# Kernel optimization log

Measured on AMD Instinct MI355X. Metric: run time of the kernel, lower is better.

## Reference

```python
import jax, jax.numpy as jnp
import numpy as np

WS = 11        # gaussian window size
SIGMA = 1.5    # gaussian sigma
L = 10.0       # val_range
SSIM_C1 = (0.01 * L) ** 2
SSIM_C2 = (0.03 * L) ** 2


def _window():
    g = jnp.exp(-((jnp.arange(WS) - WS // 2) ** 2) / (2.0 * SIGMA ** 2))
    g = g / g.sum()
    return jnp.outer(g, g).astype(jnp.float32)  # [11,11], sums to 1


def _blur(z, win):
    # depthwise 11x11 gaussian blur with VALID padding; z: [..., H, W]
    lead = z.shape[:-2]
    zf = z.reshape((-1, 1) + z.shape[-2:])
    out = jax.lax.conv_general_dilated(zf, win[None, None], (1, 1), 'VALID')
    return out.reshape(lead + out.shape[-2:])


def setup_inputs() -> dict:
    key = jax.random.key(0)
    ks = jax.random.split(key, 7)
    B, C, Fc, H, W = 8, 64, 3, 192, 192
    return {
        'x': jax.random.normal(ks[0], (B, C, H, W), jnp.float32),
        'x_feature': jax.random.normal(ks[1], (B, Fc, H, W), jnp.float32),
        'spatial_w': jax.random.normal(ks[2], (1, Fc, 3, 1), jnp.float32) * 0.1,
        'W1': jax.random.normal(ks[3], (C, C), jnp.float32) * 0.05,
        'b1': jnp.zeros((C,), jnp.float32),
        'W2': jax.random.normal(ks[4], (C, C), jnp.float32) * 0.05,
        'b2': jnp.zeros((C,), jnp.float32),
    }


def reference(x, x_feature, spatial_w, W1, b1, W2, b2):
    win = _window()
    # per-channel gaussian moments (computed once, reused across all pairs)
    mu_x = _blur(x, win)                         # [B,C,h,w]
    mu_f = _blur(x_feature, win)                 # [B,F,h,w]
    sig_x = _blur(x * x, win) - mu_x ** 2        # variance of x channels
    sig_f = _blur(x_feature * x_feature, win) - mu_f ** 2
    # all pairwise cross-covariances in one batched blur
    prod = x_feature[:, :, None] * x[:, None]    # [B,F,C,H,W]
    sig_fx = _blur(prod, win) - mu_f[:, :, None] * mu_x[:, None]
    v1 = 2.0 * sig_fx + SSIM_C2
    v2 = sig_f[:, :, None] + sig_x[:, None] + SSIM_C2
    num = (2.0 * mu_f[:, :, None] * mu_x[:, None] + SSIM_C1) * v1
    den = (mu_f[:, :, None] ** 2 + mu_x[:, None] ** 2 + SSIM_C1) * v2
    ssim_info = (num / den).mean(axis=(-2, -1))  # [B,F,C]
    # spatial gate: Conv2d(3,1,(3,1),padding=(1,0)) over [B,F,C,1]
    si4 = ssim_info[..., None]                   # [B,F,C,1]
    h = jax.lax.conv_general_dilated(si4, spatial_w, (1, 1), ((1, 1), (0, 0)))
    h = jax.nn.relu(h).reshape(x.shape[0], -1)   # [B,C]
    h = jax.nn.relu(h @ W1.T + b1) @ W2.T + b2
    return jax.nn.sigmoid(h), ssim_info
```

## Files before the change

### kernel.cpp

```cpp
#include <hip/hip_runtime.h>
#include <math.h>

#define HW 192
#define OW 182
#define NPIX (OW*OW)
#define NTILE 8
#define SSIM_C1 0.01f
#define SSIM_C2 0.09f

#define Gk0 0.0010283835f
#define Gk1 0.0075987615f
#define Gk2 0.0360007700f
#define Gk3 0.1093608000f
#define Gk4 0.2130055400f
#define Gk5 0.2660117000f

typedef float v2f __attribute__((ext_vector_type(2)));

__device__ __forceinline__ v2f vfma(float w, v2f a, v2f b) {
    return __builtin_elementwise_fma((v2f){w, w}, a, b);
}
__device__ __forceinline__ v2f vfma2(v2f w, v2f a, v2f b) {
    return __builtin_elementwise_fma(w, a, b);
}

__device__ __forceinline__ void dgauss(float g[11]) {
    float s = 0.f;
#pragma unroll
    for (int i = 0; i < 11; ++i) {
        float d = (float)(i - 5);
        g[i] = expf(-(d * d) / 4.5f);
        s += g[i];
    }
    float inv = 1.f / s;
#pragma unroll
    for (int i = 0; i < 11; ++i) g[i] *= inv;
}

__global__ __launch_bounds__(256) void muf_kernel(const float* __restrict__ xf,
                                                  float* __restrict__ muf,
                                                  float* __restrict__ sigc2f) {
    const int tile = blockIdx.x % 14;
    const int img  = blockIdx.x / 14;
    const int r0   = tile * 13;

    __shared__ float raw[23][192];
    __shared__ float hb[2][23][184];

    float g[11]; dgauss(g);
    const int t = threadIdx.x;
    const float* src = xf + (size_t)img * HW * HW;

    for (int i = t; i < 23 * 192; i += 256) {
        int rr = i / 192, col = i - rr * 192;
        raw[rr][col] = src[(r0 + rr) * HW + col];
    }
    __syncthreads();

    for (int i = t; i < 23 * OW; i += 256) {
        int rr = i / OW, co = i - rr * OW;
        float a0 = 0.f, a1 = 0.f;
#pragma unroll
        for (int k = 0; k < 11; ++k) {
            float v = raw[rr][co + k];
            float w = g[k];
            a0 += w * v;
            a1 += w * v * v;
        }
        hb[0][rr][co] = a0;
        hb[1][rr][co] = a1;
    }
    __syncthreads();

    for (int i = t; i < 13 * OW; i += 256) {
        int rr = i / OW, co = i - rr * OW;
        float m = 0.f, s2 = 0.f;
#pragma unroll
        for (int k = 0; k < 11; ++k) {
            float w = g[k];
            m  += w * hb[0][rr + k][co];
            s2 += w * hb[1][rr + k][co];
        }
        size_t o = (size_t)img * NPIX + (size_t)(r0 + rr) * OW + co;
        muf[o]    = m;
        sigc2f[o] = s2 - m * m + SSIM_C2;
    }
}

__global__ __launch_bounds__(192, 4) void ssim_kernel(const float* __restrict__ x,
                                                      const float* __restrict__ xf,
                                                      const float* __restrict__ muf,
                                                      const float* __restrict__ sigc2f,
                                                      float* __restrict__ part) {
    const float G[11] = {Gk0,Gk1,Gk2,Gk3,Gk4,Gk5,Gk4,Gk3,Gk2,Gk1,Gk0};
    const v2f WA[6] = {{G[0],0.f},{G[2],G[1]},{G[4],G[3]},{G[6],G[5]},{G[8],G[7]},{G[10],G[9]}};
    const v2f WB[6] = {{G[1],G[0]},{G[3],G[2]},{G[5],G[4]},{G[7],G[6]},{G[9],G[8]},{0.f,G[10]}};

    const int blk  = blockIdx.x;
    const int c    = blk & 63;
    const int tile = (blk >> 6) & 7;
    const int b    = blk >> 9;

    const int out0  = (tile * 182) >> 3;
    const int out1  = ((tile + 1) * 182) >> 3;
    const int n_out = out1 - out0;

    const int t    = threadIdx.x;
    const int half = (t >= 96) ? 1 : 0;
    const int u    = half ? (t - 96) : t;
    const int cu   = 2 * u;
    const bool act = (u <= 90);

    const float* xp  = x  + ((size_t)(b * 64 + c)) * HW * HW + (size_t)out0 * HW + t;
    const float* fp0 = xf + ((size_t)(b * 3 + 0)) * HW * HW + (size_t)out0 * HW + t;
    const float* fp1 = fp0 + HW * HW;
    const float* fp2 = fp1 + HW * HW;

    const float* mp = muf    + (size_t)(b * 3) * NPIX + (size_t)(out0 + half) * OW + cu;
    const float* cp = sigc2f + (size_t)(b * 3) * NPIX + (size_t)(out0 + half) * OW + cu;

    __shared__ float eb[4][5][192];
    __shared__ float red[3][3];

    v2f P01[10], P23[10];
    float P4[10];
#pragma unroll
    for (int j = 0; j < 10; ++j) { P01[j] = (v2f){0.f,0.f}; P23[j] = (v2f){0.f,0.f}; P4[j] = 0.f; }

    v2f A0 = {0.f,0.f}, A1 = {0.f,0.f}, A2 = {0.f,0.f};

    v2f eE01, eE23; float eE4;

    auto vstep = [&](float xv, float a0, float a1, float a2, bool emit) {
        v2f v01 = {xv, xv * xv};
        v2f v23 = {xv * a0, xv * a1};
        float v4 = xv * a2;
        if (emit) {
            eE01 = vfma(G[10], v01, P01[0]);
            eE23 = vfma(G[10], v23, P23[0]);
            eE4  = fmaf(G[10], v4, P4[0]);
        }
#pragma unroll
        for (int j = 0; j < 9; ++j) {
            P01[j] = vfma(G[9 - j], v01, P01[j + 1]);
            P23[j] = vfma(G[9 - j], v23, P23[j + 1]);
            P4[j]  = fmaf(G[9 - j], v4, P4[j + 1]);
        }
        P01[9] = G[0] * v01;
        P23[9] = G[0] * v23;
        P4[9]  = G[0] * v4;
    };

    auto ssim2 = [&](const v2f mux, const v2f mux2, const v2f sigc,
                     const v2f mf, const v2f cc, const v2f h, v2f& A) {
        v2f t1  = mf * mux;
        v2f sfx = h - t1;
        v2f v1s = vfma(2.f, sfx, (v2f){SSIM_C2, SSIM_C2});
        v2f n1  = vfma(2.f, t1, (v2f){SSIM_C1, SSIM_C1});
        v2f num = n1 * v1s;
        v2f qd  = vfma2(mf, mf, (v2f){SSIM_C1, SSIM_C1});
        v2f den = (qd + mux2) * (cc + sigc);
        v2f inv = {__builtin_amdgcn_rcpf(den.x), __builtin_amdgcn_rcpf(den.y)};
        A = vfma2(num, inv, A);
    };

    auto store_e = [&](int slot) {
        eb[slot][0][t] = eE01.x; eb[slot][1][t] = eE01.y;
        eb[slot][2][t] = eE23.x; eb[slot][3][t] = eE23.y;
        eb[slot][4][t] = eE4;
    };

#pragma unroll 1
    for (int r = 0; r < 10; r += 2) {
        float xA0 = xp[0],  a00 = fp0[0],  a10 = fp1[0],  a20 = fp2[0];
        float xB0 = xp[HW], b00 = fp0[HW], b10 = fp1[HW], b20 = fp2[HW];
        xp += 2 * HW; fp0 += 2 * HW; fp1 += 2 * HW; fp2 += 2 * HW;
        vstep(xA0, a00, a10, a20, false);
        vstep(xB0, b00, b10, b20, false);
    }

    const int n_pair = n_out >> 1;

    float xA = xp[0],  aA0 = fp0[0],  aA1 = fp1[0],  aA2 = fp2[0];
    float xB = xp[HW], aB0 = fp0[HW], aB1 = fp1[HW], aB2 = fp2[HW];
    xp += 2 * HW; fp0 += 2 * HW; fp1 += 2 * HW; fp2 += 2 * HW;
    float yA = xp[0],  bA0 = fp0[0],  bA1 = fp1[0],  bA2 = fp2[0];
    float yB = xp[HW], bB0 = fp0[HW], bB1 = fp1[HW], bB2 = fp2[HW];
    xp += 2 * HW; fp0 += 2 * HW; fp1 += 2 * HW; fp2 += 2 * HW;

#pragma unroll 1
    for (int p = 0; p < n_pair; ++p) {
        const int rb = 2 * p + 4;
        const int o1 = ((rb     < n_out) ? 0 : (n_out - 1 - rb)) * HW;
        const int o2 = ((rb + 1 < n_out) ? 1 : (n_out - 1 - rb)) * HW;
        const float nxA = xp[o1], nA0 = fp0[o1], nA1 = fp1[o1], nA2 = fp2[o1];
        const float nxB = xp[o2], nB0 = fp0[o2], nB1 = fp1[o2], nB2 = fp2[o2];
        xp += 2 * HW; fp0 += 2 * HW; fp1 += 2 * HW; fp2 += 2 * HW;

        v2f mf0, mf1, mf2, cc0, cc1, cc2;
        if (act) {
            mf0 = *(const v2f*)(mp);
            mf1 = *(const v2f*)(mp + NPIX);
            mf2 = *(const v2f*)(mp + 2 * NPIX);
            cc0 = *(const v2f*)(cp);
            cc1 = *(const v2f*)(cp + NPIX);
            cc2 = *(const v2f*)(cp + 2 * NPIX);
            mp += 2 * OW; cp += 2 * OW;
        }

        const int e = 2 * p;
        const int sA = e & 3, sB = (e + 1) & 3;
        vstep(xA, aA0, aA1, aA2, true);  store_e(sA);
        vstep(xB, aB0, aB1, aB2, true);  store_e(sB);
        __syncthreads();

        xA = yA;  aA0 = bA0; aA1 = bA1; aA2 = bA2;
        xB = yB;  aB0 = bB0; aB1 = bB1; aB2 = bB2;
        yA = nxA; bA0 = nA0; bA1 = nA1; bA2 = nA2;
        yB = nxB; bB0 = nB0; bB1 = nB1; bB2 = nB2;

        if (act) {
            const int sH = half ? sB : sA;
            v2f hacc[5];
#pragma unroll
            for (int f = 0; f < 5; ++f) {
                const float* ep = &eb[sH][f][cu];
                v2f a = {0.f, 0.f};
#pragma unroll
                for (int m = 0; m < 6; ++m) {
                    v2f rd = *(const v2f*)(ep + 2 * m);
                    a = vfma2(WA[m], __builtin_shufflevector(rd, rd, 0, 0), a);
                    a = vfma2(WB[m], __builtin_shufflevector(rd, rd, 1, 1), a);
                }
                hacc[f] = a;
            }
            const v2f mux  = hacc[0];
            const v2f mux2 = mux * mux;
            const v2f sigc = hacc[1] - mux2;
            ssim2(mux, mux2, sigc, mf0, cc0, hacc[2], A0);
            ssim2(mux, mux2, sigc, mf1, cc1, hacc[3], A1);
            ssim2(mux, mux2, sigc, mf2, cc2, hacc[4], A2);
        }
    }

    if (n_out & 1) {
        const int e = n_out - 1;
        vstep(xA, aA0, aA1, aA2, true);
        const int sA = e & 3;
        store_e(sA);
        __syncthreads();
        if (act && half == 0) {
            v2f mf0 = *(const v2f*)(mp);
            v2f mf1 = *(const v2f*)(mp + NPIX);
            v2f mf2 = *(const v2f*)(mp + 2 * NPIX);
            v2f cc0 = *(const v2f*)(cp);
            v2f cc1 = *(const v2f*)(cp + NPIX);
            v2f cc2 = *(const v2f*)(cp + 2 * NPIX);
            v2f hacc[5];
#pragma unroll
            for (int f = 0; f < 5; ++f) {
                const float* ep = &eb[sA][f][cu];
                v2f a = {0.f, 0.f};
#pragma unroll
                for (int m = 0; m < 6; ++m) {
                    v2f rd = *(const v2f*)(ep + 2 * m);
                    a = vfma2(WA[m], __builtin_shufflevector(rd, rd, 0, 0), a);
                    a = vfma2(WB[m], __builtin_shufflevector(rd, rd, 1, 1), a);
                }
                hacc[f] = a;
            }
            const v2f mux  = hacc[0];
            const v2f mux2 = mux * mux;
            const v2f sigc = hacc[1] - mux2;
            ssim2(mux, mux2, sigc, mf0, cc0, hacc[2], A0);
            ssim2(mux, mux2, sigc, mf1, cc1, hacc[3], A1);
            ssim2(mux, mux2, sigc, mf2, cc2, hacc[4], A2);
        }
    }

    float acc0 = A0.x + A0.y;
    float acc1 = A1.x + A1.y;
    float acc2 = A2.x + A2.y;
#pragma unroll
    for (int off = 32; off > 0; off >>= 1) {
        acc0 += __shfl_down(acc0, off);
        acc1 += __shfl_down(acc1, off);
        acc2 += __shfl_down(acc2, off);
    }
    const int wid = t >> 6, lane = t & 63;
    if (lane == 0) { red[0][wid] = acc0; red[1][wid] = acc1; red[2][wid] = acc2; }
    __syncthreads();
    if (t == 0) {
        const size_t o = (size_t)tile * 1536 + (size_t)b * 192;
        part[o +   0 + c] = red[0][0] + red[0][1] + red[0][2];
        part[o +  64 + c] = red[1][0] + red[1][1] + red[1][2];
        part[o + 128 + c] = red[2][0] + red[2][1] + red[2][2];
    }
}

__global__ __launch_bounds__(64) void gate_kernel(const float* __restrict__ part,
                                                  const float* __restrict__ sw,
                                                  const float* __restrict__ W1,
                                                  const float* __restrict__ b1,
                                                  const float* __restrict__ W2,
                                                  const float* __restrict__ b2,
                                                  float* __restrict__ out,
                                                  float* __restrict__ out_ssim) {
    const int b = blockIdx.x;
    const int c = threadIdx.x;

    __shared__ float s[3][64];
    __shared__ float h0[64];
    __shared__ float h1[64];

    const float inv = 1.f / (float)NPIX;
#pragma unroll
    for (int f = 0; f < 3; ++f) {
        const int i = b * 192 + f * 64 + c;
        float v = 0.f;
#pragma unroll
        for (int k = 0; k < NTILE; ++k) v += part[i + k * 1536];
        v *= inv;
        s[f][c] = v;
        out_ssim[i] = v;
    }
    __syncthreads();

    float a = 0.f;
#pragma unroll
    for (int f = 0; f < 3; ++f)
#pragma unroll
        for (int i = 0; i < 3; ++i) {
            int cc = c - 1 + i;
            if (cc >= 0 && cc < 64) a += sw[f * 3 + i] * s[f][cc];
        }
    h0[c] = fmaxf(a, 0.f);
    __syncthreads();

    float a1 = b1[c];
    for (int j = 0; j < 64; ++j) a1 += W1[c * 64 + j] * h0[j];
    h1[c] = fmaxf(a1, 0.f);
    __syncthreads();

    float a2 = b2[c];
    for (int j = 0; j < 64; ++j) a2 += W2[c * 64 + j] * h1[j];
    out[b * 64 + c] = 1.f / (1.f + expf(-a2));
}

extern "C" void kernel_launch(void* const* d_in, const int* in_sizes, int n_in,
                              void* d_out, int out_size, void* d_ws, size_t ws_size,
                              hipStream_t stream) {
    const float* x  = (const float*)d_in[0];
    const float* xf = (const float*)d_in[1];
    const float* sw = (const float*)d_in[2];
    const float* W1 = (const float*)d_in[3];
    const float* b1 = (const float*)d_in[4];
    const float* W2 = (const float*)d_in[5];
    const float* b2 = (const float*)d_in[6];
    float* out = (float*)d_out;

    float* muf  = (float*)d_ws;
    float* sigf = muf + 24 * NPIX;
    float* part = sigf + 24 * NPIX;

    muf_kernel <<<24 * 14,        256, 0, stream>>>(xf, muf, sigf);
    ssim_kernel<<<8 * 64 * NTILE, 192, 0, stream>>>(x, xf, muf, sigf, part);
    gate_kernel<<<8,               64, 0, stream>>>(part, sw, W1, b1, W2, b2, out, out + 512);
}
```

Baseline: 111.1 us.

## Process four output rows per barrier with an eight-slot shared ring buffer

```diff
diff --git a/kernel.cpp b/kernel.cpp
--- a/kernel.cpp
+++ b/kernel.cpp
@@ -87,7 +87,7 @@
     }
 }
 
-__global__ __launch_bounds__(192, 4) void ssim_kernel(const float* __restrict__ x,
+__global__ __launch_bounds__(192, 3) void ssim_kernel(const float* __restrict__ x,
                                                       const float* __restrict__ xf,
                                                       const float* __restrict__ muf,
                                                       const float* __restrict__ sigc2f,
@@ -119,7 +119,7 @@
     const float* mp = muf    + (size_t)(b * 3) * NPIX + (size_t)(out0 + half) * OW + cu;
     const float* cp = sigc2f + (size_t)(b * 3) * NPIX + (size_t)(out0 + half) * OW + cu;
 
-    __shared__ float eb[4][5][192];
+    __shared__ float eb[8][5][192];
     __shared__ float red[3][3];
 
     v2f P01[10], P23[10];
@@ -170,6 +170,34 @@
         eb[slot][4][t] = eE4;
     };
 
+    auto do_row = [&](int slot, int mrow) {
+        v2f mf0 = *(const v2f*)(mp + mrow);
+        v2f mf1 = *(const v2f*)(mp + mrow + NPIX);
+        v2f mf2 = *(const v2f*)(mp + mrow + 2 * NPIX);
+        v2f cc0 = *(const v2f*)(cp + mrow);
+        v2f cc1 = *(const v2f*)(cp + mrow + NPIX);
+        v2f cc2 = *(const v2f*)(cp + mrow + 2 * NPIX);
+        v2f hacc[5];
+#pragma unroll
+        for (int f = 0; f < 5; ++f) {
+            const float* ep = &eb[slot][f][cu];
+            v2f a = {0.f, 0.f};
+#pragma unroll
+            for (int m = 0; m < 6; ++m) {
+                v2f rd = *(const v2f*)(ep + 2 * m);
+                a = vfma2(WA[m], __builtin_shufflevector(rd, rd, 0, 0), a);
+                a = vfma2(WB[m], __builtin_shufflevector(rd, rd, 1, 1), a);
+            }
+            hacc[f] = a;
+        }
+        const v2f mux  = hacc[0];
+        const v2f mux2 = mux * mux;
+        const v2f sigc = hacc[1] - mux2;
+        ssim2(mux, mux2, sigc, mf0, cc0, hacc[2], A0);
+        ssim2(mux, mux2, sigc, mf1, cc1, hacc[3], A1);
+        ssim2(mux, mux2, sigc, mf2, cc2, hacc[4], A2);
+    };
+
 #pragma unroll 1
     for (int r = 0; r < 10; r += 2) {
         float xA0 = xp[0],  a00 = fp0[0],  a10 = fp1[0],  a20 = fp2[0];
@@ -179,103 +207,50 @@
         vstep(xB0, b00, b10, b20, false);
     }
 
-    const int n_pair = n_out >> 1;
-
-    float xA = xp[0],  aA0 = fp0[0],  aA1 = fp1[0],  aA2 = fp2[0];
-    float xB = xp[HW], aB0 = fp0[HW], aB1 = fp1[HW], aB2 = fp2[HW];
-    xp += 2 * HW; fp0 += 2 * HW; fp1 += 2 * HW; fp2 += 2 * HW;
-    float yA = xp[0],  bA0 = fp0[0],  bA1 = fp1[0],  bA2 = fp2[0];
-    float yB = xp[HW], bB0 = fp0[HW], bB1 = fp1[HW], bB2 = fp2[HW];
-    xp += 2 * HW; fp0 += 2 * HW; fp1 += 2 * HW; fp2 += 2 * HW;
+    const int ngrp = (n_out + 3) >> 2;
+
+    float cx[4], c0[4], c1[4], c2[4];
+#pragma unroll
+    for (int q = 0; q < 4; ++q) {
+        cx[q] = xp[q * HW]; c0[q] = fp0[q * HW];
+        c1[q] = fp1[q * HW]; c2[q] = fp2[q * HW];
+    }
+    xp += 4 * HW; fp0 += 4 * HW; fp1 += 4 * HW; fp2 += 4 * HW;
 
 #pragma unroll 1
-    for (int p = 0; p < n_pair; ++p) {
-        const int rb = 2 * p + 4;
-        const int o1 = ((rb     < n_out) ? 0 : (n_out - 1 - rb)) * HW;
-        const int o2 = ((rb + 1 < n_out) ? 1 : (n_out - 1 - rb)) * HW;
-        const float nxA = xp[o1], nA0 = fp0[o1], nA1 = fp1[o1], nA2 = fp2[o1];
-        const float nxB = xp[o2], nB0 = fp0[o2], nB1 = fp1[o2], nB2 = fp2[o2];
-        xp += 2 * HW; fp0 += 2 * HW; fp1 += 2 * HW; fp2 += 2 * HW;
-
-        v2f mf0, mf1, mf2, cc0, cc1, cc2;
-        if (act) {
-            mf0 = *(const v2f*)(mp);
-            mf1 = *(const v2f*)(mp + NPIX);
-            mf2 = *(const v2f*)(mp + 2 * NPIX);
-            cc0 = *(const v2f*)(cp);
-            cc1 = *(const v2f*)(cp + NPIX);
-            cc2 = *(const v2f*)(cp + 2 * NPIX);
-            mp += 2 * OW; cp += 2 * OW;
-        }
-
-        const int e = 2 * p;
-        const int sA = e & 3, sB = (e + 1) & 3;
-        vstep(xA, aA0, aA1, aA2, true);  store_e(sA);
-        vstep(xB, aB0, aB1, aB2, true);  store_e(sB);
+    for (int p = 0; p < ngrp; ++p) {
+        float nx[4], n0[4], n1[4], n2[4];
+        {
+            const int rb = 4 * p + 4;
+#pragma unroll
+            for (int q = 0; q < 4; ++q) {
+                const int off = (((rb + q) < n_out) ? q : (n_out - 1 - rb)) * HW;
+                nx[q] = xp[off]; n0[q] = fp0[off];
+                n1[q] = fp1[off]; n2[q] = fp2[off];
+            }
+            xp += 4 * HW; fp0 += 4 * HW; fp1 += 4 * HW; fp2 += 4 * HW;
+        }
+
+#pragma unroll
+        for (int q = 0; q < 4; ++q) {
+            const int e = 4 * p + q;
+            if (e < n_out) {
+                vstep(cx[q], c0[q], c1[q], c2[q], true);
+                store_e(e & 7);
+            }
+        }
         __syncthreads();
 
-        xA = yA;  aA0 = bA0; aA1 = bA1; aA2 = bA2;
-        xB = yB;  aB0 = bB0; aB1 = bB1; aB2 = bB2;
-        yA = nxA; bA0 = nA0; bA1 = nA1; bA2 = nA2;
-        yB = nxB; bB0 = nB0; bB1 = nB1; bB2 = nB2;
-
-        if (act) {
-            const int sH = half ? sB : sA;
-            v2f hacc[5];
-#pragma unroll
-            for (int f = 0; f < 5; ++f) {
-                const float* ep = &eb[sH][f][cu];
-                v2f a = {0.f, 0.f};
-#pragma unroll
-                for (int m = 0; m < 6; ++m) {
-                    v2f rd = *(const v2f*)(ep + 2 * m);
-                    a = vfma2(WA[m], __builtin_shufflevector(rd, rd, 0, 0), a);
-                    a = vfma2(WB[m], __builtin_shufflevector(rd, rd, 1, 1), a);
-                }
-                hacc[f] = a;
-            }
-            const v2f mux  = hacc[0];
-            const v2f mux2 = mux * mux;
-            const v2f sigc = hacc[1] - mux2;
-            ssim2(mux, mux2, sigc, mf0, cc0, hacc[2], A0);
-            ssim2(mux, mux2, sigc, mf1, cc1, hacc[3], A1);
-            ssim2(mux, mux2, sigc, mf2, cc2, hacc[4], A2);
-        }
-    }
-
-    if (n_out & 1) {
-        const int e = n_out - 1;
-        vstep(xA, aA0, aA1, aA2, true);
-        const int sA = e & 3;
-        store_e(sA);
-        __syncthreads();
-        if (act && half == 0) {
-            v2f mf0 = *(const v2f*)(mp);
-            v2f mf1 = *(const v2f*)(mp + NPIX);
-            v2f mf2 = *(const v2f*)(mp + 2 * NPIX);
-            v2f cc0 = *(const v2f*)(cp);
-            v2f cc1 = *(const v2f*)(cp + NPIX);
-            v2f cc2 = *(const v2f*)(cp + 2 * NPIX);
-            v2f hacc[5];
-#pragma unroll
-            for (int f = 0; f < 5; ++f) {
-                const float* ep = &eb[sA][f][cu];
-                v2f a = {0.f, 0.f};
-#pragma unroll
-                for (int m = 0; m < 6; ++m) {
-                    v2f rd = *(const v2f*)(ep + 2 * m);
-                    a = vfma2(WA[m], __builtin_shufflevector(rd, rd, 0, 0), a);
-                    a = vfma2(WB[m], __builtin_shufflevector(rd, rd, 1, 1), a);
-                }
-                hacc[f] = a;
-            }
-            const v2f mux  = hacc[0];
-            const v2f mux2 = mux * mux;
-            const v2f sigc = hacc[1] - mux2;
-            ssim2(mux, mux2, sigc, mf0, cc0, hacc[2], A0);
-            ssim2(mux, mux2, sigc, mf1, cc1, hacc[3], A1);
-            ssim2(mux, mux2, sigc, mf2, cc2, hacc[4], A2);
-        }
+#pragma unroll
+        for (int q = 0; q < 4; ++q) {
+            cx[q] = nx[q]; c0[q] = n0[q]; c1[q] = n1[q]; c2[q] = n2[q];
+        }
+
+        if (act) do_row((4 * p + half) & 7, 0);
+
+        if (act && (4 * p + 2 + half) < n_out) do_row((4 * p + 2 + half) & 7, 2 * OW);
+
+        mp += 4 * OW; cp += 4 * OW;
     }
 
     float acc0 = A0.x + A0.y;
```

After: 112.0 us. No clear change (+0.8%).
